# Kernel tuning notes

Measured on AMD Instinct MI355X. Metric: run time of the kernel, lower is better.

Reference implementation:

```python
import jax, jax.numpy as jnp
import numpy as np

T = 0.07  # softmax temperature from __init__
N_QUEUES = 4


def _l2norm(x, axis):
    return x / jnp.maximum(jnp.linalg.norm(x, axis=axis, keepdims=True), 1e-12)


def setup_inputs() -> dict:
    key = jax.random.key(0)
    k1, k2, k3, k4, k5, k6 = jax.random.split(key, 6)
    N, D_in, dim, K = 512, 2048, 128, 65536
    im_q = jax.random.normal(k1, (N, D_in), dtype=jnp.float32)
    im_k = jax.random.normal(k2, (N, D_in), dtype=jnp.float32)
    W_q = jax.random.normal(k3, (D_in, dim), dtype=jnp.float32) * (1.0 / np.sqrt(D_in))
    W_k = jax.random.normal(k4, (D_in, dim), dtype=jnp.float32) * (1.0 / np.sqrt(D_in))
    queues = jax.random.normal(k5, (N_QUEUES, dim, K), dtype=jnp.float32)
    queues = _l2norm(queues, axis=1)  # normalize along feature dim, as in __init__
    label = jax.random.randint(k6, (N,), 0, 4, dtype=jnp.int32)
    return {"im_q": im_q, "im_k": im_k, "W_q": W_q, "W_k": W_k,
            "queues": queues, "label": label}


def reference(im_q, im_k, W_q, W_k, queues, label):
    # encoder_q / encoder_k abstracted as linear projections
    q = _l2norm(im_q @ W_q, axis=1)                      # [N, C]
    k = _l2norm(im_k @ W_k, axis=1)                      # [N, C] (no_grad in original)
    l_pos = jnp.einsum('nc,nc->n', q, k)[:, None]        # [N, 1]
    # per-sample queue routing: queue index = (label - 1) % 4
    route = jnp.mod(label - 1, N_QUEUES)                 # [N]
    onehot = jax.nn.one_hot(route, N_QUEUES, dtype=q.dtype)  # [N, G]
    # l_neg[n, k] = sum_c q[n, c] * queues[route[n], c, k], as grouped matmul
    l_neg = jnp.einsum('ngc,gck->nk', q[:, None, :] * onehot[:, :, None], queues)  # [N, K]
    logits = jnp.concatenate([l_pos, l_neg], axis=1) / T  # [N, 1+K]
    labels = jnp.zeros(logits.shape[0], dtype=jnp.int32)
    return logits, labels
```

## Files before the change

### kernel.cpp

```cpp
#include <hip/hip_runtime.h>

typedef short short8 __attribute__((ext_vector_type(8)));
typedef float floatx4 __attribute__((ext_vector_type(4)));

__device__ __forceinline__ unsigned short f2bf(float f) {
  unsigned u = __float_as_uint(f);
  u += 0x7FFFu + ((u >> 16) & 1u);
  return (unsigned short)(u >> 16);
}

__global__ __launch_bounds__(256) void proj_partial(
    const float* __restrict__ im_q, const float* __restrict__ im_k,
    const float* __restrict__ Wq, const float* __restrict__ Wk,
    float* __restrict__ part, int* __restrict__ cnt) {
  __shared__ float imS[32 * 260];
  const int t = threadIdx.x;
  if (blockIdx.x == 0 && blockIdx.y == 0 && blockIdx.z == 0 && t < 4) cnt[t] = 0;
  const int which = blockIdx.z;
  const float* __restrict__ im = which ? im_k : im_q;
  const float* __restrict__ W  = which ? Wk : Wq;
  const int d0 = blockIdx.x * 256;
  const int row0 = blockIdx.y * 32;
  {
    const int dd0 = (t & 63) * 4;
    const int rb = t >> 6;
#pragma unroll
    for (int p = 0; p < 8; ++p) {
      const int r = rb + p * 4;
      const float4 v = *(const float4*)(im + (size_t)(row0 + r) * 2048 + d0 + dd0);
      *(float4*)(imS + r * 260 + dd0) = v;
    }
  }
  __syncthreads();
  const int c4 = (t & 31) * 4;
  const int r4 = (t >> 5) * 4;
  float acc[4][4] = {};
  const float* __restrict__ Wp = W + (size_t)d0 * 128 + c4;
#pragma unroll 4
  for (int d = 0; d < 256; ++d) {
    const float4 w = *(const float4*)(Wp + (size_t)d * 128);
    float a[4];
#pragma unroll
    for (int rr = 0; rr < 4; ++rr) a[rr] = imS[(r4 + rr) * 260 + d];
#pragma unroll
    for (int rr = 0; rr < 4; ++rr) {
      acc[rr][0] += a[rr] * w.x;
      acc[rr][1] += a[rr] * w.y;
      acc[rr][2] += a[rr] * w.z;
      acc[rr][3] += a[rr] * w.w;
    }
  }
#pragma unroll
  for (int rr = 0; rr < 4; ++rr) {
    float4 v = make_float4(acc[rr][0], acc[rr][1], acc[rr][2], acc[rr][3]);
    *(float4*)(part + ((size_t)(which * 8 + blockIdx.x) * 512 + row0 + r4 + rr) * 128 + c4) = v;
  }
}

__global__ __launch_bounds__(128) void finalize(
    const float* __restrict__ part, const int* __restrict__ label,
    unsigned short* __restrict__ qbf, int* __restrict__ cnt,
    int* __restrict__ rows, float* __restrict__ out) {
  const int n = blockIdx.x, c = threadIdx.x;
  float qraw = 0.f, kraw = 0.f;
#pragma unroll
  for (int ch = 0; ch < 8; ++ch) {
    qraw += part[((size_t)ch * 512 + n) * 128 + c];
    kraw += part[((size_t)(8 + ch) * 512 + n) * 128 + c];
  }
  float sq = qraw * qraw, sk = kraw * kraw, dt = qraw * kraw;
#pragma unroll
  for (int off = 32; off > 0; off >>= 1) {
    sq += __shfl_down(sq, off, 64);
    sk += __shfl_down(sk, off, 64);
    dt += __shfl_down(dt, off, 64);
  }
  __shared__ float sh[3][2];
  const int lane = c & 63, wv = c >> 6;
  if (lane == 0) { sh[0][wv] = sq; sh[1][wv] = sk; sh[2][wv] = dt; }
  __syncthreads();
  const float tsq = sh[0][0] + sh[0][1];
  const float tsk = sh[1][0] + sh[1][1];
  const float tdt = sh[2][0] + sh[2][1];
  const float nq = fmaxf(sqrtf(tsq), 1e-12f);
  const float nk = fmaxf(sqrtf(tsk), 1e-12f);
  qbf[n * 128 + c] = f2bf(qraw / nq);
  if (c == 0) {
    out[(size_t)n * 65537] = tdt / (nq * nk) * (1.0f / 0.07f);
    ((int*)out)[(size_t)512 * 65537 + n] = 0;
    int g = ((label[n] - 1) % 4 + 4) % 4;
    int pos = atomicAdd(cnt + g, 1);
    rows[g * 512 + pos] = n;
  }
}

__global__ __launch_bounds__(256) void moco_lneg(
    const float* __restrict__ queues, const unsigned short* __restrict__ qbf,
    const int* __restrict__ cnt, const int* __restrict__ rows,
    float* __restrict__ out) {
  __shared__ unsigned short Bs[128 * 130];
  __shared__ unsigned short Qs[128 * 130];
  __shared__ int rowsS[128];
  const int g = blockIdx.y;
  const int Mg = cnt[g];
  if (Mg == 0) return;
  const int t = threadIdx.x;
  const int j0 = blockIdx.x * 128;
  {
    const int j = t & 127;
    const int cb = (t >> 7) * 64;
    const float* __restrict__ qb = queues + (size_t)g * 128 * 65536 + j0 + j;
#pragma unroll 8
    for (int p = 0; p < 32; ++p) {
      const int c = cb + p * 2;
      const float f0 = qb[(size_t)c * 65536];
      const float f1 = qb[(size_t)(c + 1) * 65536];
      const unsigned u = (unsigned)f2bf(f0) | ((unsigned)f2bf(f1) << 16);
      *(unsigned*)(Bs + j * 130 + c) = u;
    }
  }
  const int lane = t & 63, wave = t >> 6;
  const int qd = lane >> 4, l16 = lane & 15;
  const float invT = 1.0f / 0.07f;
  for (int chunk0 = 0; chunk0 < Mg; chunk0 += 128) {
    __syncthreads();
    const int valid = min(Mg - chunk0, 128);
    if (t < 128) rowsS[t] = (t < valid) ? rows[g * 512 + chunk0 + t] : 0;
    {
      const int m = t >> 1, half = (t & 1) * 64;
      if (m < valid) {
        const int rg = rows[g * 512 + chunk0 + m];
        const unsigned* __restrict__ src = (const unsigned*)(qbf + rg * 128 + half);
#pragma unroll
        for (int i = 0; i < 32; ++i)
          *(unsigned*)(Qs + m * 130 + half + i * 2) = src[i];
      } else {
#pragma unroll
        for (int i = 0; i < 32; ++i)
          *(unsigned*)(Qs + m * 130 + half + i * 2) = 0u;
      }
    }
    __syncthreads();
    floatx4 acc[8][2];
#pragma unroll
    for (int rb = 0; rb < 8; ++rb) {
      floatx4 z = {0.f, 0.f, 0.f, 0.f};
      acc[rb][0] = z; acc[rb][1] = z;
    }
#pragma unroll
    for (int kk = 0; kk < 4; ++kk) {
      const int k0 = kk * 32 + qd * 8;
      short8 bfrag[2];
#pragma unroll
      for (int s = 0; s < 2; ++s) {
        const unsigned* p = (const unsigned*)(Bs + ((wave * 2 + s) * 16 + l16) * 130 + k0);
        unsigned* d = (unsigned*)&bfrag[s];
        d[0] = p[0]; d[1] = p[1]; d[2] = p[2]; d[3] = p[3];
      }
#pragma unroll
      for (int rb = 0; rb < 8; ++rb) {
        const unsigned* p = (const unsigned*)(Qs + (rb * 16 + l16) * 130 + k0);
        short8 afrag;
        unsigned* d = (unsigned*)&afrag;
        d[0] = p[0]; d[1] = p[1]; d[2] = p[2]; d[3] = p[3];
        acc[rb][0] = __builtin_amdgcn_mfma_f32_16x16x32_bf16(afrag, bfrag[0], acc[rb][0], 0, 0, 0);
        acc[rb][1] = __builtin_amdgcn_mfma_f32_16x16x32_bf16(afrag, bfrag[1], acc[rb][1], 0, 0, 0);
      }
    }
#pragma unroll
    for (int rb = 0; rb < 8; ++rb) {
#pragma unroll
      for (int r = 0; r < 4; ++r) {
        const int ml = rb * 16 + qd * 4 + r;
        if (ml < valid) {
          const size_t base = (size_t)rowsS[ml] * 65537 + 1 + j0;
#pragma unroll
          for (int s = 0; s < 2; ++s)
            out[base + (wave * 2 + s) * 16 + l16] = acc[rb][s][r] * invT;
        }
      }
    }
  }
}

extern "C" void kernel_launch(void* const* d_in, const int* in_sizes, int n_in,
                              void* d_out, int out_size, void* d_ws, size_t ws_size,
                              hipStream_t stream) {
  const float* im_q   = (const float*)d_in[0];
  const float* im_k   = (const float*)d_in[1];
  const float* Wq     = (const float*)d_in[2];
  const float* Wk     = (const float*)d_in[3];
  const float* queues = (const float*)d_in[4];
  const int*   label  = (const int*)d_in[5];
  float* out = (float*)d_out;

  char* ws = (char*)d_ws;
  float* part = (float*)ws;
  unsigned short* qbf = (unsigned short*)(ws + (4u << 20));
  int* cnt  = (int*)(ws + (4u << 20) + (128u << 10));
  int* rows = cnt + 4;

  proj_partial<<<dim3(8, 16, 2), 256, 0, stream>>>(im_q, im_k, Wq, Wk, part, cnt);
  finalize<<<512, 128, 0, stream>>>(part, label, qbf, cnt, rows, out);
  moco_lneg<<<dim3(512, 4), 256, 0, stream>>>(queues, qbf, cnt, rows, out);
}
```

Baseline: 315.4 us.

## Prepack routed q fragments into MFMA layout and shrink projection tiles

Adds a qpack kernel that gathers the bf16 q rows per queue group into a layout matching the MFMA A-fragment lane order. moco_lneg then loads A fragments straight from global memory instead of staging them through shared memory, which removes the per-chunk Qs fill and its barriers. The kernel also skips row blocks that have no valid rows, pads Bs rows to 136 so 16-byte LDS reads work, and raises wave priority around the MFMA loop. proj_partial moves to 512 threads with 16 rows per block and one row per thread, which means more blocks and less register tiling; Apack reuses the workspace region that held part.

```diff
diff --git a/kernel.cpp b/kernel.cpp
--- a/kernel.cpp
+++ b/kernel.cpp
@@ -9,52 +9,39 @@
   return (unsigned short)(u >> 16);
 }
 
-__global__ __launch_bounds__(256) void proj_partial(
+__global__ __launch_bounds__(512, 4) void proj_partial(
     const float* __restrict__ im_q, const float* __restrict__ im_k,
     const float* __restrict__ Wq, const float* __restrict__ Wk,
     float* __restrict__ part, int* __restrict__ cnt) {
-  __shared__ float imS[32 * 260];
+  __shared__ float imS[16 * 260];
   const int t = threadIdx.x;
   if (blockIdx.x == 0 && blockIdx.y == 0 && blockIdx.z == 0 && t < 4) cnt[t] = 0;
   const int which = blockIdx.z;
   const float* __restrict__ im = which ? im_k : im_q;
   const float* __restrict__ W  = which ? Wk : Wq;
   const int d0 = blockIdx.x * 256;
-  const int row0 = blockIdx.y * 32;
-  {
-    const int dd0 = (t & 63) * 4;
-    const int rb = t >> 6;
-#pragma unroll
-    for (int p = 0; p < 8; ++p) {
-      const int r = rb + p * 4;
-      const float4 v = *(const float4*)(im + (size_t)(row0 + r) * 2048 + d0 + dd0);
-      *(float4*)(imS + r * 260 + dd0) = v;
-    }
+  const int row0 = blockIdx.y * 16;
+#pragma unroll
+  for (int p = 0; p < 2; ++p) {
+    const int idx = t + p * 512;
+    const int r = idx >> 6;
+    const int dd = (idx & 63) * 4;
+    *(float4*)(imS + r * 260 + dd) =
+        *(const float4*)(im + (size_t)(row0 + r) * 2048 + d0 + dd);
   }
   __syncthreads();
   const int c4 = (t & 31) * 4;
-  const int r4 = (t >> 5) * 4;
-  float acc[4][4] = {};
+  const int r  = t >> 5;
+  float acc0 = 0.f, acc1 = 0.f, acc2 = 0.f, acc3 = 0.f;
   const float* __restrict__ Wp = W + (size_t)d0 * 128 + c4;
-#pragma unroll 4
+#pragma unroll 8
   for (int d = 0; d < 256; ++d) {
     const float4 w = *(const float4*)(Wp + (size_t)d * 128);
-    float a[4];
-#pragma unroll
-    for (int rr = 0; rr < 4; ++rr) a[rr] = imS[(r4 + rr) * 260 + d];
-#pragma unroll
-    for (int rr = 0; rr < 4; ++rr) {
-      acc[rr][0] += a[rr] * w.x;
-      acc[rr][1] += a[rr] * w.y;
-      acc[rr][2] += a[rr] * w.z;
-      acc[rr][3] += a[rr] * w.w;
-    }
-  }
-#pragma unroll
-  for (int rr = 0; rr < 4; ++rr) {
-    float4 v = make_float4(acc[rr][0], acc[rr][1], acc[rr][2], acc[rr][3]);
-    *(float4*)(part + ((size_t)(which * 8 + blockIdx.x) * 512 + row0 + r4 + rr) * 128 + c4) = v;
-  }
+    const float a = imS[r * 260 + d];
+    acc0 += a * w.x; acc1 += a * w.y; acc2 += a * w.z; acc3 += a * w.w;
+  }
+  *(float4*)(part + ((size_t)(which * 8 + blockIdx.x) * 512 + row0 + r) * 128 + c4) =
+      make_float4(acc0, acc1, acc2, acc3);
 }
 
 __global__ __launch_bounds__(128) void finalize(
@@ -94,13 +81,35 @@
   }
 }
 
-__global__ __launch_bounds__(256) void moco_lneg(
-    const float* __restrict__ queues, const unsigned short* __restrict__ qbf,
+__global__ __launch_bounds__(256) void qpack(
+    const unsigned short* __restrict__ qbf, const int* __restrict__ cnt,
+    const int* __restrict__ rows, unsigned short* __restrict__ Apack) {
+  const int g = blockIdx.x >> 2, ch = blockIdx.x & 3;
+  const int Mg = cnt[g];
+  const int t = threadIdx.x;
+#pragma unroll
+  for (int w = 0; w < 8; ++w) {
+    const int slot = w * 256 + t;
+    const int kk = slot >> 9;
+    const int rb = (slot >> 6) & 7;
+    const int lane = slot & 63;
+    const int l16 = lane & 15, qd = lane >> 4;
+    const int m = ch * 128 + rb * 16 + l16;
+    uint4 v = make_uint4(0u, 0u, 0u, 0u);
+    if (m < Mg) {
+      const int n = rows[g * 512 + m];
+      v = *(const uint4*)(qbf + (size_t)n * 128 + kk * 32 + qd * 8);
+    }
+    *(uint4*)(Apack + ((size_t)blockIdx.x * 2048 + slot) * 8) = v;
+  }
+}
+
+__global__ __launch_bounds__(256, 4) void moco_lneg(
+    const float* __restrict__ queues, const unsigned short* __restrict__ Apack,
     const int* __restrict__ cnt, const int* __restrict__ rows,
     float* __restrict__ out) {
-  __shared__ unsigned short Bs[128 * 130];
-  __shared__ unsigned short Qs[128 * 130];
-  __shared__ int rowsS[128];
+  __shared__ __align__(16) unsigned short Bs[128 * 136];
+  __shared__ int rowsS[512];
   const int g = blockIdx.y;
   const int Mg = cnt[g];
   if (Mg == 0) return;
@@ -116,67 +125,52 @@
       const float f0 = qb[(size_t)c * 65536];
       const float f1 = qb[(size_t)(c + 1) * 65536];
       const unsigned u = (unsigned)f2bf(f0) | ((unsigned)f2bf(f1) << 16);
-      *(unsigned*)(Bs + j * 130 + c) = u;
-    }
-  }
+      *(unsigned*)(Bs + j * 136 + c) = u;
+    }
+  }
+  for (int i = t; i < 512; i += 256) rowsS[i] = rows[g * 512 + i];
+  __syncthreads();
   const int lane = t & 63, wave = t >> 6;
   const int qd = lane >> 4, l16 = lane & 15;
   const float invT = 1.0f / 0.07f;
-  for (int chunk0 = 0; chunk0 < Mg; chunk0 += 128) {
-    __syncthreads();
-    const int valid = min(Mg - chunk0, 128);
-    if (t < 128) rowsS[t] = (t < valid) ? rows[g * 512 + chunk0 + t] : 0;
-    {
-      const int m = t >> 1, half = (t & 1) * 64;
-      if (m < valid) {
-        const int rg = rows[g * 512 + chunk0 + m];
-        const unsigned* __restrict__ src = (const unsigned*)(qbf + rg * 128 + half);
-#pragma unroll
-        for (int i = 0; i < 32; ++i)
-          *(unsigned*)(Qs + m * 130 + half + i * 2) = src[i];
-      } else {
-#pragma unroll
-        for (int i = 0; i < 32; ++i)
-          *(unsigned*)(Qs + m * 130 + half + i * 2) = 0u;
-      }
-    }
-    __syncthreads();
+  const int nch = (Mg + 127) >> 7;
+  const unsigned short* __restrict__ Ag = Apack + (size_t)g * 4 * 16384 + lane * 8;
+  for (int ch = 0; ch < nch; ++ch) {
+    const int valid = min(Mg - ch * 128, 128);
+    const unsigned short* __restrict__ Ab = Ag + (size_t)ch * 16384;
     floatx4 acc[8][2];
 #pragma unroll
     for (int rb = 0; rb < 8; ++rb) {
       floatx4 z = {0.f, 0.f, 0.f, 0.f};
       acc[rb][0] = z; acc[rb][1] = z;
     }
+    __builtin_amdgcn_s_setprio(1);
 #pragma unroll
     for (int kk = 0; kk < 4; ++kk) {
       const int k0 = kk * 32 + qd * 8;
-      short8 bfrag[2];
-#pragma unroll
-      for (int s = 0; s < 2; ++s) {
-        const unsigned* p = (const unsigned*)(Bs + ((wave * 2 + s) * 16 + l16) * 130 + k0);
-        unsigned* d = (unsigned*)&bfrag[s];
-        d[0] = p[0]; d[1] = p[1]; d[2] = p[2]; d[3] = p[3];
+      const short8 bfrag0 = *(const short8*)&Bs[((wave * 2 + 0) * 16 + l16) * 136 + k0];
+      const short8 bfrag1 = *(const short8*)&Bs[((wave * 2 + 1) * 16 + l16) * 136 + k0];
+#pragma unroll
+      for (int rb = 0; rb < 8; ++rb) {
+        if (rb * 16 < valid) {
+          const short8 afrag = *(const short8*)(Ab + kk * 4096 + rb * 512);
+          acc[rb][0] = __builtin_amdgcn_mfma_f32_16x16x32_bf16(afrag, bfrag0, acc[rb][0], 0, 0, 0);
+          acc[rb][1] = __builtin_amdgcn_mfma_f32_16x16x32_bf16(afrag, bfrag1, acc[rb][1], 0, 0, 0);
+        }
       }
-#pragma unroll
-      for (int rb = 0; rb < 8; ++rb) {
-        const unsigned* p = (const unsigned*)(Qs + (rb * 16 + l16) * 130 + k0);
-        short8 afrag;
-        unsigned* d = (unsigned*)&afrag;
-        d[0] = p[0]; d[1] = p[1]; d[2] = p[2]; d[3] = p[3];
-        acc[rb][0] = __builtin_amdgcn_mfma_f32_16x16x32_bf16(afrag, bfrag[0], acc[rb][0], 0, 0, 0);
-        acc[rb][1] = __builtin_amdgcn_mfma_f32_16x16x32_bf16(afrag, bfrag[1], acc[rb][1], 0, 0, 0);
-      }
-    }
+    }
+    __builtin_amdgcn_s_setprio(0);
 #pragma unroll
     for (int rb = 0; rb < 8; ++rb) {
-#pragma unroll
-      for (int r = 0; r < 4; ++r) {
-        const int ml = rb * 16 + qd * 4 + r;
-        if (ml < valid) {
-          const size_t base = (size_t)rowsS[ml] * 65537 + 1 + j0;
-#pragma unroll
-          for (int s = 0; s < 2; ++s)
-            out[base + (wave * 2 + s) * 16 + l16] = acc[rb][s][r] * invT;
+      if (rb * 16 < valid) {
+#pragma unroll
+        for (int r = 0; r < 4; ++r) {
+          const int ml = rb * 16 + qd * 4 + r;
+          if (ml < valid) {
+            const size_t base = (size_t)rowsS[ch * 128 + ml] * 65537 + 1 + j0;
+            out[base + (wave * 2 + 0) * 16 + l16] = acc[rb][0][r] * invT;
+            out[base + (wave * 2 + 1) * 16 + l16] = acc[rb][1][r] * invT;
+          }
         }
       }
     }
@@ -199,8 +193,10 @@
   unsigned short* qbf = (unsigned short*)(ws + (4u << 20));
   int* cnt  = (int*)(ws + (4u << 20) + (128u << 10));
   int* rows = cnt + 4;
-
-  proj_partial<<<dim3(8, 16, 2), 256, 0, stream>>>(im_q, im_k, Wq, Wk, part, cnt);
+  unsigned short* Apack = (unsigned short*)ws;
+
+  proj_partial<<<dim3(8, 32, 2), 512, 0, stream>>>(im_q, im_k, Wq, Wk, part, cnt);
   finalize<<<512, 128, 0, stream>>>(part, label, qbf, cnt, rows, out);
-  moco_lneg<<<dim3(512, 4), 256, 0, stream>>>(queues, qbf, cnt, rows, out);
-}
+  qpack<<<16, 256, 0, stream>>>(qbf, cnt, rows, Apack);
+  moco_lneg<<<dim3(512, 4), 256, 0, stream>>>(queues, Apack, cnt, rows, out);
+}
```

Result: slower. 322.8 us (+2.4%).
